# Performance work log

Hardware: AMD Instinct MI355X
Metric: run time of the kernel (lower is better)

Reference implementation:

```python
import jax, jax.numpy as jnp
import numpy as np

B, T, E, H, HD, FF = 2, 2048, 1024, 16, 64, 4096
LN_EPS = 1e-5


def _ln(x, g, b):
    mu = jnp.mean(x, axis=-1, keepdims=True)
    var = jnp.var(x, axis=-1, keepdims=True)
    return (x - mu) * jax.lax.rsqrt(var + LN_EPS) * g + b


def setup_inputs() -> dict:
    key = jax.random.key(0)
    ks = jax.random.split(key, 8)
    s = 0.02
    return {
        "x": jax.random.normal(ks[0], (B, T, E), jnp.float32),
        "Wq": jax.random.normal(ks[1], (H, E, HD), jnp.float32) * s,
        "Wk": jax.random.normal(ks[2], (H, E, HD), jnp.float32) * s,
        "Wv": jax.random.normal(ks[3], (H, E, HD), jnp.float32) * s,
        "Wproj": jax.random.normal(ks[4], (E, E), jnp.float32) * s,
        "bproj": jnp.zeros((E,), jnp.float32),
        "W1": jax.random.normal(ks[5], (E, FF), jnp.float32) * s,
        "b1": jnp.zeros((FF,), jnp.float32),
        "W2": jax.random.normal(ks[6], (FF, E), jnp.float32) * s,
        "b2": jnp.zeros((E,), jnp.float32),
        "g1": jnp.ones((E,), jnp.float32),
        "be1": jnp.zeros((E,), jnp.float32),
        "g2": jnp.ones((E,), jnp.float32),
        "be2": jnp.zeros((E,), jnp.float32),
    }


def reference(x, Wq, Wk, Wv, Wproj, bproj, W1, b1, W2, b2, g1, be1, g2, be2):
    # --- pre-LN multi-head causal self-attention (dropout = eval/identity) ---
    h = _ln(x, g1, be1)  # [B,T,E]
    q = jnp.einsum('btd,hde->bhte', h, Wq)  # [B,H,T,HD]
    k = jnp.einsum('btd,hde->bhte', h, Wk)
    v = jnp.einsum('btd,hde->bhte', h, Wv)
    # NOTE: original code scales by C**-0.5 where C = embedding_dim (not head_size)
    scale = E ** (-0.5)
    wei = jnp.einsum('bhqe,bhke->bhqk', q, k) * scale  # [B,H,T,T]
    causal = jnp.tril(jnp.ones((T, T), dtype=bool))
    wei = jnp.where(causal, wei, -jnp.inf)
    attn = jax.nn.softmax(wei, axis=-1)
    o = jnp.einsum('bhqk,bhke->bhqe', attn, v)  # [B,H,T,HD]
    o = o.transpose(0, 2, 1, 3).reshape(B, T, E)  # concat heads
    o = o @ Wproj + bproj
    x = x + o
    # --- ReLU FFN ---
    h2 = _ln(x, g2, be2)
    f = jax.nn.relu(h2 @ W1 + b1) @ W2 + b2
    return x + f
```

## Files before the change

### kernel.cpp

```cpp
#include <hip/hip_runtime.h>
#include <hip/hip_bf16.h>
#include <stdint.h>

#define T_SEQ 2048
#define E_DIM 1024
#define H_NUM 16
#define HD_DIM 64
#define FF_DIM 4096
#define B_NUM 2
#define N_TOK (B_NUM * T_SEQ)

typedef unsigned short ushort_t;
typedef __bf16 bf16x8 __attribute__((ext_vector_type(8)));
typedef float f32x4 __attribute__((ext_vector_type(4)));

__device__ __forceinline__ float bf2f(ushort_t u) {
    return __uint_as_float(((unsigned)u) << 16);
}
__device__ __forceinline__ ushort_t f2bf(float f) {
    unsigned u = __float_as_uint(f);
    u += 0x7fffu + ((u >> 16) & 1u);
    return (ushort_t)(u >> 16);
}

__device__ __forceinline__ void async_copy16(const ushort_t* g, ushort_t* l) {
    __builtin_amdgcn_global_load_lds(
        (__attribute__((address_space(1))) uint32_t*)(ushort_t*)g,
        (__attribute__((address_space(3))) uint32_t*)l, 16, 0, 0);
}

__global__ __launch_bounds__(256) void ln_kernel(const float* __restrict__ x,
                                                 const float* __restrict__ g,
                                                 const float* __restrict__ be,
                                                 ushort_t* __restrict__ out) {
    __shared__ float red[8];
    const int row = blockIdx.x, tid = threadIdx.x;
    const float* xr = x + (size_t)row * E_DIM;
    float4 v = ((const float4*)xr)[tid];
    float s = v.x + v.y + v.z + v.w;
    float sq = v.x * v.x + v.y * v.y + v.z * v.z + v.w * v.w;
    for (int off = 32; off; off >>= 1) {
        s += __shfl_xor(s, off);
        sq += __shfl_xor(sq, off);
    }
    const int wid = tid >> 6, lane = tid & 63;
    if (lane == 0) { red[wid] = s; red[4 + wid] = sq; }
    __syncthreads();
    s = red[0] + red[1] + red[2] + red[3];
    sq = red[4] + red[5] + red[6] + red[7];
    const float mean = s * (1.0f / E_DIM);
    const float var = sq * (1.0f / E_DIM) - mean * mean;
    const float rstd = rsqrtf(var + 1e-5f);
    float4 gv = ((const float4*)g)[tid];
    float4 bv = ((const float4*)be)[tid];
    unsigned o0 = f2bf((v.x - mean) * rstd * gv.x + bv.x);
    unsigned o1 = f2bf((v.y - mean) * rstd * gv.y + bv.y);
    unsigned o2 = f2bf((v.z - mean) * rstd * gv.z + bv.z);
    unsigned o3 = f2bf((v.w - mean) * rstd * gv.w + bv.w);
    uint2 w;
    w.x = o0 | (o1 << 16);
    w.y = o2 | (o3 << 16);
    ((uint2*)(out + (size_t)row * E_DIM))[tid] = w;
}

__global__ __launch_bounds__(256) void transpose_kernel(const float* __restrict__ in,
                                                        ushort_t* __restrict__ out,
                                                        int R, int C) {
    __shared__ ushort_t tile[32][33];
    const int c0 = blockIdx.x * 32, r0 = blockIdx.y * 32;
    const int tx = threadIdx.x, ty = threadIdx.y;
#pragma unroll
    for (int i = 0; i < 32; i += 8) tile[ty + i][tx] = f2bf(in[(size_t)(r0 + ty + i) * C + (c0 + tx)]);
    __syncthreads();
#pragma unroll
    for (int i = 0; i < 32; i += 8) out[(size_t)(c0 + ty + i) * R + (r0 + tx)] = tile[tx][ty + i];
}

__global__ __launch_bounds__(256) void transpose_qkv_kernel(const float* __restrict__ Wq,
                                                            const float* __restrict__ Wk,
                                                            const float* __restrict__ Wv,
                                                            ushort_t* __restrict__ outT) {
    __shared__ ushort_t tile[32][33];
    const int z = blockIdx.z, m = z >> 4, hh = z & 15;
    const float* in = ((m == 0) ? Wq : ((m == 1) ? Wk : Wv)) + (size_t)hh * E_DIM * HD_DIM;
    ushort_t* out = outT + (size_t)(m * E_DIM + hh * HD_DIM) * E_DIM;
    const int c0 = blockIdx.x * 32, r0 = blockIdx.y * 32;
    const int tx = threadIdx.x, ty = threadIdx.y;
#pragma unroll
    for (int i = 0; i < 32; i += 8) tile[ty + i][tx] = f2bf(in[(size_t)(r0 + ty + i) * HD_DIM + (c0 + tx)]);
    __syncthreads();
#pragma unroll
    for (int i = 0; i < 32; i += 8) out[(size_t)(c0 + ty + i) * E_DIM + (r0 + tx)] = tile[tx][ty + i];
}

template <int MODE>
__global__ __launch_bounds__(256) void gemm_bt(const ushort_t* __restrict__ A,
                                               const ushort_t* __restrict__ BT,
                                               const float* __restrict__ bias,
                                               const float* __restrict__ resid,
                                               void* __restrict__ C0,
                                               ushort_t* __restrict__ C1,
                                               ushort_t* __restrict__ C2,
                                               int M, int N, int K) {
    __shared__ __align__(16) ushort_t lds_a[2][128 * 32];
    __shared__ __align__(16) ushort_t lds_b[2][128 * 32];
    const int tid = threadIdx.x;
    const int id = blockIdx.y * gridDim.x + blockIdx.x;
    const int band = id & 7, within = id >> 3;
    const int rpb = gridDim.y >> 3;
    const int by = band * rpb + (within % rpb);
    const int bx = within / rpb;
    const int m0 = by * 128, n0 = bx * 128;
    const int wave = tid >> 6, lane = tid & 63;
    const int wm = (wave >> 1) * 64, wn = (wave & 1) * 64;
    const int quad = lane >> 4, l16 = lane & 15;
    f32x4 acc[4][4] = {};
    const int ci = tid, ci2 = 256 + tid;
    const int r1 = ci >> 2, kc1 = ci & 3;
    const int r2 = ci2 >> 2, kc2 = ci2 & 3;

    const int nk = K >> 5;
    async_copy16(A + (size_t)(m0 + r1) * K + kc1 * 8, &lds_a[0][ci * 8]);
    async_copy16(BT + (size_t)(n0 + r1) * K + kc1 * 8, &lds_b[0][ci * 8]);
    async_copy16(A + (size_t)(m0 + r2) * K + kc2 * 8, &lds_a[0][ci2 * 8]);
    async_copy16(BT + (size_t)(n0 + r2) * K + kc2 * 8, &lds_b[0][ci2 * 8]);

#pragma unroll 1
    for (int kt = 0; kt < nk; ++kt) {
        __syncthreads();
        if (kt + 1 < nk) {
            const int k1 = (kt + 1) << 5;
            ushort_t* la = lds_a[(kt + 1) & 1];
            ushort_t* lb = lds_b[(kt + 1) & 1];
            async_copy16(A + (size_t)(m0 + r1) * K + (k1 + kc1 * 8), &la[ci * 8]);
            async_copy16(BT + (size_t)(n0 + r1) * K + (k1 + kc1 * 8), &lb[ci * 8]);
            async_copy16(A + (size_t)(m0 + r2) * K + (k1 + kc2 * 8), &la[ci2 * 8]);
            async_copy16(BT + (size_t)(n0 + r2) * K + (k1 + kc2 * 8), &lb[ci2 * 8]);
        }
        const ushort_t* la = lds_a[kt & 1];
        const ushort_t* lb = lds_b[kt & 1];
        bf16x8 af[4], bfr[4];
#pragma unroll
        for (int i = 0; i < 4; i++) af[i] = *(const bf16x8*)&la[(wm + i * 16 + l16) * 32 + quad * 8];
#pragma unroll
        for (int i = 0; i < 4; i++) bfr[i] = *(const bf16x8*)&lb[(wn + i * 16 + l16) * 32 + quad * 8];
#pragma unroll
        for (int im = 0; im < 4; im++)
#pragma unroll
            for (int in = 0; in < 4; in++)
                acc[im][in] = __builtin_amdgcn_mfma_f32_16x16x32_bf16(af[im], bfr[in], acc[im][in], 0, 0, 0);
    }

#pragma unroll
    for (int im = 0; im < 4; im++) {
#pragma unroll
        for (int in = 0; in < 4; in++) {
            const int col = n0 + wn + in * 16 + l16;
            float bv = (MODE != 0) ? bias[col] : 0.0f;
#pragma unroll
            for (int r = 0; r < 4; r++) {
                const int row = m0 + wm + im * 16 + quad * 4 + r;
                float v = acc[im][in][r] + bv;
                if (MODE == 2) v = fmaxf(v, 0.0f);
                if (MODE == 1) v += resid[(size_t)row * N + col];
                if (MODE == 0) {
                    const int mat = col >> 10, c = col & 1023, hh = c >> 6, d = c & 63;
                    const int bb = row >> 11, tt = row & 2047;
                    const int bh = bb * H_NUM + hh;
                    size_t idx;
                    ushort_t* dst;
                    if (mat == 0) {
                        idx = ((((size_t)bh * 32 + (tt >> 6)) * 8 + (d >> 3)) * 64 + (tt & 63)) * 8 + (d & 7);
                        dst = (ushort_t*)C0;
                        v *= 0.0450842048f;
                    } else if (mat == 1) {
                        idx = ((((size_t)bh * 32 + (tt >> 6)) * 8 + (d >> 3)) * 64 + (tt & 63)) * 8 + (d & 7);
                        dst = C1;
                    } else {
                        idx = ((((size_t)bh * 32 + (tt >> 6)) * 8 + ((tt & 63) >> 3)) * 64 + d) * 8 + (tt & 7);
                        dst = C2;
                    }
                    dst[idx] = f2bf(v);
                } else if (MODE == 1) {
                    ((float*)C0)[(size_t)row * N + col] = v;
                } else {
                    ((ushort_t*)C0)[(size_t)row * N + col] = f2bf(v);
                }
            }
        }
    }
    (void)M;
}

__global__ __launch_bounds__(256) void attn_flash(const ushort_t* __restrict__ qP,
                                                  const ushort_t* __restrict__ kP,
                                                  const ushort_t* __restrict__ vP,
                                                  ushort_t* __restrict__ o) {
    __shared__ __align__(16) ushort_t K_lds[2][4096];
    __shared__ __align__(16) ushort_t V_lds[2][4096];
    __shared__ __align__(16) ushort_t P_lds[4 * 16 * 72];
    const int p = blockIdx.x, h = blockIdx.y, b = blockIdx.z;
    const int bh = b * H_NUM + h;
    const int tid = threadIdx.x;
    const int wave = tid >> 6, lane = tid & 63;
    const int quad = lane >> 4, l16 = lane & 15;
    const int qrow0 = wave * 16;
    ushort_t* Pw = &P_lds[wave * 16 * 72];
    const ushort_t* kt_base = kP + (size_t)bh * 32 * 4096;
    const ushort_t* vt_base = vP + (size_t)bh * 32 * 4096;
    bf16x8 onesf;
#pragma unroll
    for (int j = 0; j < 8; ++j) onesf[j] = (__bf16)1.0f;

#pragma unroll 1
    for (int phase = 0; phase < 2; ++phase) {
        const int qt = (phase == 0) ? (31 - p) : p;
        const ushort_t* qbase = qP + ((size_t)bh * 32 + qt) * 4096;
        bf16x8 qf[2];
#pragma unroll
        for (int kk = 0; kk < 2; kk++)
            qf[kk] = *(const bf16x8*)&qbase[((kk * 4 + quad) * 64 + qrow0 + l16) * 8];
        f32x4 oacc[4] = {};
        f32x4 lacc = {};
        const int nkt = qt + 1;
        __syncthreads();
#pragma unroll
        for (int it = 0; it < 2; ++it) {
            const int ci = it * 256 + tid;
            async_copy16(kt_base + ci * 8, &K_lds[0][ci * 8]);
            async_copy16(vt_base + ci * 8, &V_lds[0][ci * 8]);
        }
#pragma unroll 1
        for (int kt = 0; kt < nkt; ++kt) {
            __syncthreads();
            if (kt + 1 < nkt) {
                const ushort_t* kn = kt_base + (size_t)(kt + 1) * 4096;
                const ushort_t* vn = vt_base + (size_t)(kt + 1) * 4096;
                ushort_t* kd = K_lds[(kt + 1) & 1];
                ushort_t* vd = V_lds[(kt + 1) & 1];
#pragma unroll
                for (int it = 0; it < 2; ++it) {
                    const int ci = it * 256 + tid;
                    async_copy16(kn + ci * 8, &kd[ci * 8]);
                    async_copy16(vn + ci * 8, &vd[ci * 8]);
                }
            }
            const ushort_t* Kb = K_lds[kt & 1];
            const ushort_t* Vb = V_lds[kt & 1];
            f32x4 sacc[4] = {};
#pragma unroll
            for (int kk = 0; kk < 2; kk++) {
                bf16x8 bfr[4];
#pragma unroll
                for (int in = 0; in < 4; in++)
                    bfr[in] = *(const bf16x8*)&Kb[(kk * 4 + quad) * 512 + (in * 16 + l16) * 8];
#pragma unroll
                for (int in = 0; in < 4; in++)
                    sacc[in] = __builtin_amdgcn_mfma_f32_16x16x32_bf16(qf[kk], bfr[in], sacc[in], 0, 0, 0);
            }
#pragma unroll
            for (int in = 0; in < 4; in++) {
                f32x4 sv = sacc[in];
                if (kt == qt) {
                    const int jc = in * 16 + l16;
#pragma unroll
                    for (int r = 0; r < 4; r++)
                        if (jc > qrow0 + quad * 4 + r) sv[r] = -3.0e38f;
                }
#pragma unroll
                for (int r = 0; r < 4; r++) {
                    const float e = exp2f(sv[r]);
                    Pw[(quad * 4 + r) * 72 + in * 16 + l16] =
                        (ushort_t)(__float_as_uint(e) >> 16);
                }
            }
#pragma unroll
            for (int kk = 0; kk < 2; kk++) {
                bf16x8 pf = *(const bf16x8*)&Pw[l16 * 72 + kk * 32 + quad * 8];
                lacc = __builtin_amdgcn_mfma_f32_16x16x32_bf16(pf, onesf, lacc, 0, 0, 0);
#pragma unroll
                for (int in = 0; in < 4; in++) {
                    bf16x8 vf = *(const bf16x8*)&Vb[(kk * 4 + quad) * 512 + (in * 16 + l16) * 8];
                    oacc[in] = __builtin_amdgcn_mfma_f32_16x16x32_bf16(pf, vf, oacc[in], 0, 0, 0);
                }
            }
        }
#pragma unroll
        for (int r = 0; r < 4; r++) {
            const float inv = 1.0f / lacc[r];
            const int trow = qt * 64 + qrow0 + quad * 4 + r;
#pragma unroll
            for (int in = 0; in < 4; in++) {
                o[(size_t)(b * T_SEQ + trow) * E_DIM + h * HD_DIM + in * 16 + l16] =
                    f2bf(oacc[in][r] * inv);
            }
        }
    }
}

extern "C" void kernel_launch(void* const* d_in, const int* in_sizes, int n_in,
                              void* d_out, int out_size, void* d_ws, size_t ws_size,
                              hipStream_t stream) {
    const float* x = (const float*)d_in[0];
    const float* Wq = (const float*)d_in[1];
    const float* Wk = (const float*)d_in[2];
    const float* Wv = (const float*)d_in[3];
    const float* Wproj = (const float*)d_in[4];
    const float* bproj = (const float*)d_in[5];
    const float* W1 = (const float*)d_in[6];
    const float* b1 = (const float*)d_in[7];
    const float* W2 = (const float*)d_in[8];
    const float* b2 = (const float*)d_in[9];
    const float* g1 = (const float*)d_in[10];
    const float* be1 = (const float*)d_in[11];
    const float* g2 = (const float*)d_in[12];
    const float* be2 = (const float*)d_in[13];

    char* ws = (char*)d_ws;
    const size_t MB = 1024 * 1024;
    ushort_t* W2T    = (ushort_t*)(ws + 0 * MB);
    float*    x1     = (float*)   (ws + 8 * MB);
    ushort_t* W1T    = (ushort_t*)(ws + 24 * MB);
    ushort_t* WprojT = (ushort_t*)(ws + 32 * MB);
    ushort_t* hln    = (ushort_t*)(ws + 34 * MB);
    ushort_t* ocat   = hln;
    ushort_t* WqkvT  = (ushort_t*)(ws + 42 * MB);
    ushort_t* qP     = (ushort_t*)(ws + 48 * MB);
    ushort_t* kP     = (ushort_t*)(ws + 56 * MB);
    ushort_t* vP     = (ushort_t*)(ws + 64 * MB);
    ushort_t* h2     = (ushort_t*)(ws + 72 * MB);
    ushort_t* f1     = (ushort_t*)(ws + 34 * MB);
    (void)ws_size; (void)in_sizes; (void)n_in; (void)out_size;

    const dim3 tb(32, 8, 1);
    transpose_qkv_kernel<<<dim3(2, 32, 48), tb, 0, stream>>>(Wq, Wk, Wv, WqkvT);
    transpose_kernel<<<dim3(32, 32, 1), tb, 0, stream>>>(Wproj, WprojT, E_DIM, E_DIM);
    transpose_kernel<<<dim3(128, 32, 1), tb, 0, stream>>>(W1, W1T, E_DIM, FF_DIM);
    transpose_kernel<<<dim3(32, 128, 1), tb, 0, stream>>>(W2, W2T, FF_DIM, E_DIM);

    ln_kernel<<<N_TOK, 256, 0, stream>>>(x, g1, be1, hln);
    gemm_bt<0><<<dim3(24, 32), 256, 0, stream>>>(hln, WqkvT, nullptr, nullptr,
                                                 qP, kP, vP, N_TOK, 3 * E_DIM, E_DIM);
    attn_flash<<<dim3(16, 16, 2), 256, 0, stream>>>(qP, kP, vP, ocat);
    gemm_bt<1><<<dim3(8, 32), 256, 0, stream>>>(ocat, WprojT, bproj, x,
                                                x1, nullptr, nullptr, N_TOK, E_DIM, E_DIM);
    ln_kernel<<<N_TOK, 256, 0, stream>>>(x1, g2, be2, h2);
    gemm_bt<2><<<dim3(32, 32), 256, 0, stream>>>(h2, W1T, b1, nullptr,
                                                 f1, nullptr, nullptr, N_TOK, FF_DIM, E_DIM);
    gemm_bt<1><<<dim3(8, 32), 256, 0, stream>>>(f1, W2T, b2, x1,
                                                (float*)d_out, nullptr, nullptr, N_TOK, E_DIM, FF_DIM);
}
```

Before: 380.3 us.

## Split-K the projection and FFN-down GEMMs and fuse reduction with LayerNorm

The two N=1024 GEMMs (attention projection and W2) now run split-K by 2 over blockIdx.z, doubling the grid from 256 to 512 blocks so more CUs stay busy. Each half writes bf16 partials, and new reduce kernels add both partials to the bias and residual. The reduction after the projection is fused with the second LayerNorm, replacing the separate ln_kernel. This costs extra partial-buffer traffic, an extra launch for the output reduce, and bf16 rounding of the partial sums.

```diff
diff --git a/kernel.cpp b/kernel.cpp
--- a/kernel.cpp
+++ b/kernel.cpp
@@ -22,6 +22,8 @@
     u += 0x7fffu + ((u >> 16) & 1u);
     return (ushort_t)(u >> 16);
 }
+__device__ __forceinline__ float bflo(unsigned u) { return __uint_as_float(u << 16); }
+__device__ __forceinline__ float bfhi(unsigned u) { return __uint_as_float(u & 0xffff0000u); }
 
 __device__ __forceinline__ void async_copy16(const ushort_t* g, ushort_t* l) {
     __builtin_amdgcn_global_load_lds(
@@ -63,6 +65,70 @@
     ((uint2*)(out + (size_t)row * E_DIM))[tid] = w;
 }
 
+__global__ __launch_bounds__(256) void reduce_ln_kernel(const ushort_t* __restrict__ p0,
+                                                        const ushort_t* __restrict__ p1,
+                                                        const float* __restrict__ x,
+                                                        const float* __restrict__ bias,
+                                                        const float* __restrict__ g,
+                                                        const float* __restrict__ be,
+                                                        float* __restrict__ x1,
+                                                        ushort_t* __restrict__ h2) {
+    __shared__ float red[8];
+    const int row = blockIdx.x, tid = threadIdx.x;
+    uint2 u0 = ((const uint2*)(p0 + (size_t)row * E_DIM))[tid];
+    uint2 u1 = ((const uint2*)(p1 + (size_t)row * E_DIM))[tid];
+    float4 xv = ((const float4*)(x + (size_t)row * E_DIM))[tid];
+    float4 bv = ((const float4*)bias)[tid];
+    float4 v;
+    v.x = xv.x + bv.x + bflo(u0.x) + bflo(u1.x);
+    v.y = xv.y + bv.y + bfhi(u0.x) + bfhi(u1.x);
+    v.z = xv.z + bv.z + bflo(u0.y) + bflo(u1.y);
+    v.w = xv.w + bv.w + bfhi(u0.y) + bfhi(u1.y);
+    ((float4*)(x1 + (size_t)row * E_DIM))[tid] = v;
+    float s = v.x + v.y + v.z + v.w;
+    float sq = v.x * v.x + v.y * v.y + v.z * v.z + v.w * v.w;
+    for (int off = 32; off; off >>= 1) {
+        s += __shfl_xor(s, off);
+        sq += __shfl_xor(sq, off);
+    }
+    const int wid = tid >> 6, lane = tid & 63;
+    if (lane == 0) { red[wid] = s; red[4 + wid] = sq; }
+    __syncthreads();
+    s = red[0] + red[1] + red[2] + red[3];
+    sq = red[4] + red[5] + red[6] + red[7];
+    const float mean = s * (1.0f / E_DIM);
+    const float var = sq * (1.0f / E_DIM) - mean * mean;
+    const float rstd = rsqrtf(var + 1e-5f);
+    float4 gv = ((const float4*)g)[tid];
+    float4 ev = ((const float4*)be)[tid];
+    unsigned o0 = f2bf((v.x - mean) * rstd * gv.x + ev.x);
+    unsigned o1 = f2bf((v.y - mean) * rstd * gv.y + ev.y);
+    unsigned o2 = f2bf((v.z - mean) * rstd * gv.z + ev.z);
+    unsigned o3 = f2bf((v.w - mean) * rstd * gv.w + ev.w);
+    uint2 w;
+    w.x = o0 | (o1 << 16);
+    w.y = o2 | (o3 << 16);
+    ((uint2*)(h2 + (size_t)row * E_DIM))[tid] = w;
+}
+
+__global__ __launch_bounds__(256) void reduce_out_kernel(const ushort_t* __restrict__ p0,
+                                                         const ushort_t* __restrict__ p1,
+                                                         const float* __restrict__ x1,
+                                                         const float* __restrict__ bias,
+                                                         float* __restrict__ out) {
+    const int row = blockIdx.x, tid = threadIdx.x;
+    uint2 u0 = ((const uint2*)(p0 + (size_t)row * E_DIM))[tid];
+    uint2 u1 = ((const uint2*)(p1 + (size_t)row * E_DIM))[tid];
+    float4 xv = ((const float4*)(x1 + (size_t)row * E_DIM))[tid];
+    float4 bv = ((const float4*)bias)[tid];
+    float4 v;
+    v.x = xv.x + bv.x + bflo(u0.x) + bflo(u1.x);
+    v.y = xv.y + bv.y + bfhi(u0.x) + bfhi(u1.x);
+    v.z = xv.z + bv.z + bflo(u0.y) + bflo(u1.y);
+    v.w = xv.w + bv.w + bfhi(u0.y) + bfhi(u1.y);
+    ((float4*)(out + (size_t)row * E_DIM))[tid] = v;
+}
+
 __global__ __launch_bounds__(256) void transpose_kernel(const float* __restrict__ in,
                                                         ushort_t* __restrict__ out,
                                                         int R, int C) {
@@ -101,7 +167,7 @@
                                                void* __restrict__ C0,
                                                ushort_t* __restrict__ C1,
                                                ushort_t* __restrict__ C2,
-                                               int M, int N, int K) {
+                                               int M, int N, int K, int lda) {
     __shared__ __align__(16) ushort_t lds_a[2][128 * 32];
     __shared__ __align__(16) ushort_t lds_b[2][128 * 32];
     const int tid = threadIdx.x;
@@ -111,6 +177,7 @@
     const int by = band * rpb + (within % rpb);
     const int bx = within / rpb;
     const int m0 = by * 128, n0 = bx * 128;
+    const int koff = blockIdx.z * K;
     const int wave = tid >> 6, lane = tid & 63;
     const int wm = (wave >> 1) * 64, wn = (wave & 1) * 64;
     const int quad = lane >> 4, l16 = lane & 15;
@@ -120,22 +187,22 @@
     const int r2 = ci2 >> 2, kc2 = ci2 & 3;
 
     const int nk = K >> 5;
-    async_copy16(A + (size_t)(m0 + r1) * K + kc1 * 8, &lds_a[0][ci * 8]);
-    async_copy16(BT + (size_t)(n0 + r1) * K + kc1 * 8, &lds_b[0][ci * 8]);
-    async_copy16(A + (size_t)(m0 + r2) * K + kc2 * 8, &lds_a[0][ci2 * 8]);
-    async_copy16(BT + (size_t)(n0 + r2) * K + kc2 * 8, &lds_b[0][ci2 * 8]);
+    async_copy16(A + (size_t)(m0 + r1) * lda + (koff + kc1 * 8), &lds_a[0][ci * 8]);
+    async_copy16(BT + (size_t)(n0 + r1) * lda + (koff + kc1 * 8), &lds_b[0][ci * 8]);
+    async_copy16(A + (size_t)(m0 + r2) * lda + (koff + kc2 * 8), &lds_a[0][ci2 * 8]);
+    async_copy16(BT + (size_t)(n0 + r2) * lda + (koff + kc2 * 8), &lds_b[0][ci2 * 8]);
 
 #pragma unroll 1
     for (int kt = 0; kt < nk; ++kt) {
         __syncthreads();
         if (kt + 1 < nk) {
-            const int k1 = (kt + 1) << 5;
+            const int k1 = koff + ((kt + 1) << 5);
             ushort_t* la = lds_a[(kt + 1) & 1];
             ushort_t* lb = lds_b[(kt + 1) & 1];
-            async_copy16(A + (size_t)(m0 + r1) * K + (k1 + kc1 * 8), &la[ci * 8]);
-            async_copy16(BT + (size_t)(n0 + r1) * K + (k1 + kc1 * 8), &lb[ci * 8]);
-            async_copy16(A + (size_t)(m0 + r2) * K + (k1 + kc2 * 8), &la[ci2 * 8]);
-            async_copy16(BT + (size_t)(n0 + r2) * K + (k1 + kc2 * 8), &lb[ci2 * 8]);
+            async_copy16(A + (size_t)(m0 + r1) * lda + (k1 + kc1 * 8), &la[ci * 8]);
+            async_copy16(BT + (size_t)(n0 + r1) * lda + (k1 + kc1 * 8), &lb[ci * 8]);
+            async_copy16(A + (size_t)(m0 + r2) * lda + (k1 + kc2 * 8), &la[ci2 * 8]);
+            async_copy16(BT + (size_t)(n0 + r2) * lda + (k1 + kc2 * 8), &lb[ci2 * 8]);
         }
         const ushort_t* la = lds_a[kt & 1];
         const ushort_t* lb = lds_b[kt & 1];
@@ -151,12 +218,14 @@
                 acc[im][in] = __builtin_amdgcn_mfma_f32_16x16x32_bf16(af[im], bfr[in], acc[im][in], 0, 0, 0);
     }
 
+    ushort_t* pc = nullptr;
+    if (MODE == 3) pc = (blockIdx.z == 0) ? (ushort_t*)C0 : C1;
 #pragma unroll
     for (int im = 0; im < 4; im++) {
 #pragma unroll
         for (int in = 0; in < 4; in++) {
             const int col = n0 + wn + in * 16 + l16;
-            float bv = (MODE != 0) ? bias[col] : 0.0f;
+            float bv = (MODE == 1 || MODE == 2) ? bias[col] : 0.0f;
 #pragma unroll
             for (int r = 0; r < 4; r++) {
                 const int row = m0 + wm + im * 16 + quad * 4 + r;
@@ -183,8 +252,10 @@
                     dst[idx] = f2bf(v);
                 } else if (MODE == 1) {
                     ((float*)C0)[(size_t)row * N + col] = v;
+                } else if (MODE == 2) {
+                    ((ushort_t*)C0)[(size_t)row * N + col] = f2bf(v);
                 } else {
-                    ((ushort_t*)C0)[(size_t)row * N + col] = f2bf(v);
+                    pc[(size_t)row * N + col] = f2bf(v);
                 }
             }
         }
@@ -330,6 +401,10 @@
     ushort_t* vP     = (ushort_t*)(ws + 64 * MB);
     ushort_t* h2     = (ushort_t*)(ws + 72 * MB);
     ushort_t* f1     = (ushort_t*)(ws + 34 * MB);
+    ushort_t* pp0    = (ushort_t*)(ws + 48 * MB);
+    ushort_t* pp1    = (ushort_t*)(ws + 56 * MB);
+    ushort_t* fp0    = (ushort_t*)(ws + 66 * MB);
+    ushort_t* fp1    = (ushort_t*)(ws + 24 * MB);
     (void)ws_size; (void)in_sizes; (void)n_in; (void)out_size;
 
     const dim3 tb(32, 8, 1);
@@ -340,13 +415,14 @@
 
     ln_kernel<<<N_TOK, 256, 0, stream>>>(x, g1, be1, hln);
     gemm_bt<0><<<dim3(24, 32), 256, 0, stream>>>(hln, WqkvT, nullptr, nullptr,
-                                                 qP, kP, vP, N_TOK, 3 * E_DIM, E_DIM);
+                                                 qP, kP, vP, N_TOK, 3 * E_DIM, E_DIM, E_DIM);
     attn_flash<<<dim3(16, 16, 2), 256, 0, stream>>>(qP, kP, vP, ocat);
-    gemm_bt<1><<<dim3(8, 32), 256, 0, stream>>>(ocat, WprojT, bproj, x,
-                                                x1, nullptr, nullptr, N_TOK, E_DIM, E_DIM);
-    ln_kernel<<<N_TOK, 256, 0, stream>>>(x1, g2, be2, h2);
+    gemm_bt<3><<<dim3(8, 32, 2), 256, 0, stream>>>(ocat, WprojT, nullptr, nullptr,
+                                                   pp0, pp1, nullptr, N_TOK, E_DIM, 512, E_DIM);
+    reduce_ln_kernel<<<N_TOK, 256, 0, stream>>>(pp0, pp1, x, bproj, g2, be2, x1, h2);
     gemm_bt<2><<<dim3(32, 32), 256, 0, stream>>>(h2, W1T, b1, nullptr,
-                                                 f1, nullptr, nullptr, N_TOK, FF_DIM, E_DIM);
-    gemm_bt<1><<<dim3(8, 32), 256, 0, stream>>>(f1, W2T, b2, x1,
-                                                (float*)d_out, nullptr, nullptr, N_TOK, E_DIM, FF_DIM);
-}
+                                                 f1, nullptr, nullptr, N_TOK, FF_DIM, E_DIM, E_DIM);
+    gemm_bt<3><<<dim3(8, 32, 2), 256, 0, stream>>>(f1, W2T, nullptr, nullptr,
+                                                   fp0, fp1, nullptr, N_TOK, E_DIM, 2048, FF_DIM);
+    reduce_out_kernel<<<N_TOK, 256, 0, stream>>>(fp0, fp1, x1, b2, (float*)d_out);
+}
```

After: 353.5 us. -7.0%, faster.
